# Performance work log

Hardware: AMD Instinct MI355X
Metric: run time of the kernel (lower is better)

## Reference

```python
import jax, jax.numpy as jnp
from jax import lax
import numpy as np

B, T, DIM = 2, 2048, 2048
H, Dk, Dv, K = 16, 128, 128, 4
QD, VD = H * Dk, H * Dv


def setup_inputs() -> dict:
    key = jax.random.key(0)
    ks = jax.random.split(key, 16)
    s = 0.02
    f32 = jnp.float32
    return {
        "x": jax.random.normal(ks[0], (B, T, DIM), f32),
        "Wq": jax.random.normal(ks[1], (DIM, QD), f32) * s,
        "Wk": jax.random.normal(ks[2], (DIM, QD), f32) * s,
        "Wv": jax.random.normal(ks[3], (DIM, VD), f32) * s,
        "Wo": jax.random.normal(ks[4], (VD, DIM), f32) * s,
        "Wg": jax.random.normal(ks[5], (DIM, VD), f32) * s,
        "qconv_w": jax.random.normal(ks[6], (QD, 1, K), f32) * s,
        "qconv_b": jax.random.normal(ks[7], (QD,), f32) * s,
        "kconv_w": jax.random.normal(ks[8], (QD, 1, K), f32) * s,
        "kconv_b": jax.random.normal(ks[9], (QD,), f32) * s,
        "vconv_w": jax.random.normal(ks[10], (VD, 1, K), f32) * s,
        "vconv_b": jax.random.normal(ks[11], (VD,), f32) * s,
        "beta": jax.random.normal(ks[12], (H,), f32) * 0.1,
        "A_log": jax.random.normal(ks[13], (H,), f32) * 0.1,
    }


def _causal_conv(x, w, b):
    # x: (B, T, C); depthwise causal conv, kernel K, left-pad K-1 (matches
    # Conv1d(padding=K-1, groups=C) followed by trimming the last K-1 steps).
    C = x.shape[-1]
    xp = jnp.pad(x, ((0, 0), (K - 1, 0), (0, 0))).transpose(0, 2, 1)  # (B,C,T+K-1)
    y = lax.conv_general_dilated(
        xp, w, window_strides=(1,), padding='VALID',
        feature_group_count=C, dimension_numbers=('NCH', 'OIH', 'NCH'))
    return y.transpose(0, 2, 1) + b  # (B, T, C)


def reference(x, Wq, Wk, Wv, Wo, Wg, qconv_w, qconv_b, kconv_w, kconv_b,
              vconv_w, vconv_b, beta, A_log):
    q = jax.nn.silu(_causal_conv(x @ Wq, qconv_w, qconv_b)).reshape(B, T, H, Dk)
    k = jax.nn.silu(_causal_conv(x @ Wk, kconv_w, kconv_b)).reshape(B, T, H, Dk)
    v = _causal_conv(x @ Wv, vconv_w, vconv_b).reshape(B, T, H, Dv)

    # F.normalize(k, p=2, dim=-1) with eps clamp
    k = k / jnp.maximum(jnp.linalg.norm(k, axis=-1, keepdims=True), 1e-12)

    decay = jax.nn.sigmoid(A_log)[None, :, None, None]  # (1,H,1,1)
    bet = jax.nn.sigmoid(beta)[None, :, None, None]     # (1,H,1,1)

    def step(state, qkv_t):
        q_t, k_t, v_t = qkv_t  # (B,H,Dk), (B,H,Dk), (B,H,Dv)
        state = decay * state + bet * (v_t[..., :, None] * k_t[..., None, :])
        out_t = jnp.einsum('bhvd,bhd->bhv', state, q_t)
        return state, out_t

    qT = q.transpose(1, 0, 2, 3)  # (T,B,H,Dk)
    kT = k.transpose(1, 0, 2, 3)
    vT = v.transpose(1, 0, 2, 3)
    state0 = jnp.zeros((B, H, Dv, Dk), x.dtype)
    _, outs = lax.scan(step, state0, (qT, kT, vT))  # outs: (T,B,H,Dv)

    out = outs.transpose(1, 0, 2, 3).reshape(B, T, VD)
    out = out * jax.nn.sigmoid(x @ Wg)  # output gate
    return out @ Wo
```

## Files before the change

### kernel.cpp

```cpp
#include <hip/hip_runtime.h>
#include <math.h>

#define B_   2
#define T_   2048
#define DIM_ 2048
#define H_   16

typedef __attribute__((ext_vector_type(8))) _Float16 half8;
typedef __attribute__((ext_vector_type(4))) float f32x4;

__device__ __forceinline__ float sigmoidf_(float x) { return 1.0f / (1.0f + __expf(-x)); }

__device__ __forceinline__ void gload16(const _Float16* g, _Float16* l) {
    __builtin_amdgcn_global_load_lds((const __attribute__((address_space(1))) void*)g,
                                     (__attribute__((address_space(3))) void*)l, 16, 0, 0);
}

#define VMW(n) asm volatile("s_waitcnt vmcnt(" #n ")" ::: "memory")

__device__ __forceinline__ int tsw(int row, int s) {
    return row * 72 + ((((s >> 3) ^ ((row >> 3) & 7)) << 3) | (s & 7));
}
__device__ __forceinline__ int tswb(int row, int sb) {
    return row * 72 + (((sb ^ ((row >> 3) & 7)) << 3));
}

__global__ __launch_bounds__(256) void prep(const float* __restrict__ W0,
                                            const float* __restrict__ W1,
                                            const float* __restrict__ W2,
                                            const float* __restrict__ W3,
                                            const float* __restrict__ W4,
                                            _Float16* __restrict__ wbase,
                                            const float* __restrict__ x,
                                            _Float16* __restrict__ xh)
{
    const int z = blockIdx.z;
    if (z == 5) {
        size_t blk = ((size_t)blockIdx.y * 32 + blockIdx.x) * 8192;
#pragma unroll
        for (int j = 0; j < 4; ++j) {
            size_t i = blk + (size_t)j * 2048 + (size_t)threadIdx.x * 8;
            float4 a = *(const float4*)(x + i);
            float4 b = *(const float4*)(x + i + 4);
            half8 h;
            h[0] = (_Float16)a.x; h[1] = (_Float16)a.y; h[2] = (_Float16)a.z; h[3] = (_Float16)a.w;
            h[4] = (_Float16)b.x; h[5] = (_Float16)b.y; h[6] = (_Float16)b.z; h[7] = (_Float16)b.w;
            *(half8*)(xh + i) = h;
        }
        return;
    }
    __shared__ float t[64][65];
    const float* W = z == 0 ? W0 : z == 1 ? W1 : z == 2 ? W2 : z == 3 ? W3 : W4;
    _Float16* Wt = wbase + (size_t)z * DIM_ * DIM_;
    const int c = threadIdx.x & 63;
    const int r0 = threadIdx.x >> 6;
    const int n0 = blockIdx.x * 64, k0 = blockIdx.y * 64;
#pragma unroll
    for (int i = 0; i < 16; ++i) {
        int r = i * 4 + r0;
        t[r][c] = W[(size_t)(k0 + r) * DIM_ + n0 + c];
    }
    __syncthreads();
#pragma unroll
    for (int i = 0; i < 16; ++i) {
        int r = i * 4 + r0;
        Wt[(size_t)(n0 + r) * DIM_ + k0 + c] = (_Float16)t[c][r];
    }
}

template <int BM>
__global__ __launch_bounds__(512, 1) void gemm8ph(const _Float16* __restrict__ A,
                                                  const _Float16* __restrict__ Bt,
                                                  _Float16* __restrict__ C0, _Float16* __restrict__ C1,
                                                  _Float16* __restrict__ C2, _Float16* __restrict__ C3,
                                                  int K, int nx, int cpx)
{
    constexpr int MF  = BM / 32;
    constexpr int AQ  = MF / 4;
    constexpr int ASZ = BM * 64;
    constexpr int DSZ = (BM + 256) * 64;
    __shared__ _Float16 lds[2 * DSZ];

    const int tid = threadIdx.x;
    const int lane = tid & 63, w = tid >> 6;
    const int wr = w >> 2, wc = w & 3;
    const int l15 = lane & 15, l16 = lane >> 4;

    const int bid = blockIdx.x;
    const int swz = (bid & 7) * cpx + (bid >> 3);
    const int bm = (swz / nx) * BM, bn = (swz % nx) * 256;

    const int r0 = tid >> 3;
    const int c0 = ((tid & 7) ^ (r0 & 7)) * 8;
    const _Float16* Ab = A + (size_t)(bm + r0) * K + c0;
    const _Float16* Bb = Bt + (size_t)(bn + r0) * K + c0;

#define STAGE_A(d, kt) do { _Pragma("unroll")                                    \
    for (int u = 0; u < BM / 64; ++u)                                            \
        gload16(Ab + (size_t)(u * 64) * K + (size_t)(kt) * 64,                   \
                lds + (d) * DSZ + u * 4096 + tid * 8); } while (0)
#define STAGE_B(d, h, kt) do {                                                   \
    gload16(Bb + (size_t)((h) * 128) * K + (size_t)(kt) * 64,                    \
            lds + (d) * DSZ + ASZ + (h) * 8192 + tid * 8);                       \
    gload16(Bb + (size_t)((h) * 128 + 64) * K + (size_t)(kt) * 64,               \
            lds + (d) * DSZ + ASZ + (h) * 8192 + 4096 + tid * 8); } while (0)

    int aoff[MF][2], boff[4][2];
#pragma unroll
    for (int m = 0; m < MF; ++m) {
        int R = wr * (BM / 2) + m * 16 + l15;
#pragma unroll
        for (int ks = 0; ks < 2; ++ks)
            aoff[m][ks] = R * 64 + (((ks * 4 + l16) ^ (R & 7)) * 8);
    }
#pragma unroll
    for (int n = 0; n < 4; ++n) {
        int R = wc * 64 + n * 16 + l15;
#pragma unroll
        for (int ks = 0; ks < 2; ++ks)
            boff[n][ks] = ASZ + R * 64 + (((ks * 4 + l16) ^ (R & 7)) * 8);
    }

    f32x4 acc[MF][4] = {};
    half8 bfr[4][2];
    const int nj = K >> 7;

    STAGE_A(0, 0);
    STAGE_B(0, 0, 0); STAGE_B(0, 1, 0);
    STAGE_B(1, 0, 1); STAGE_B(1, 1, 1);
    VMW(4);
    __builtin_amdgcn_s_barrier();
    __builtin_amdgcn_sched_barrier(0);

#define PH(TT, Q, STAGECODE, VMCODE) do {                                        \
    const int dB_ = (TT) * DSZ;                                                  \
    half8 af_[AQ][2];                                                            \
    if ((Q) == 0) {                                                              \
        _Pragma("unroll") for (int n_ = 0; n_ < 4; ++n_)                         \
        _Pragma("unroll") for (int ks_ = 0; ks_ < 2; ++ks_)                      \
            bfr[n_][ks_] = *(const half8*)(lds + dB_ + boff[n_][ks_]);           \
    }                                                                            \
    _Pragma("unroll") for (int a_ = 0; a_ < AQ; ++a_)                            \
    _Pragma("unroll") for (int ks_ = 0; ks_ < 2; ++ks_)                          \
        af_[a_][ks_] = *(const half8*)(lds + dB_ + aoff[(Q) * AQ + a_][ks_]);    \
    STAGECODE;                                                                   \
    __builtin_amdgcn_s_barrier();                                                \
    asm volatile("s_waitcnt lgkmcnt(0)" ::: "memory");                           \
    __builtin_amdgcn_sched_barrier(0);                                           \
    __builtin_amdgcn_s_setprio(1);                                               \
    _Pragma("unroll") for (int ks_ = 0; ks_ < 2; ++ks_)                          \
    _Pragma("unroll") for (int a_ = 0; a_ < AQ; ++a_)                            \
    _Pragma("unroll") for (int n_ = 0; n_ < 4; ++n_)                             \
        acc[(Q) * AQ + a_][n_] = __builtin_amdgcn_mfma_f32_16x16x32_f16(         \
            af_[a_][ks_], bfr[n_][ks_], acc[(Q) * AQ + a_][n_], 0, 0, 0);        \
    __builtin_amdgcn_s_setprio(0);                                               \
    __builtin_amdgcn_sched_barrier(0);                                           \
    VMCODE;                                                                      \
    __builtin_amdgcn_s_barrier();                                                \
} while (0)

    for (int j = 0; j < nj; ++j) {
        const bool pf = (j + 1 < nj);
        const int t1 = 2 * j + 1, tn0 = 2 * j + 2, tn1 = 2 * j + 3;
        PH(0, 0, { STAGE_A(1, t1); }, {});
        PH(0, 1, { if (pf) STAGE_B(0, 0, tn0); }, {});
        PH(0, 2, { if (pf) STAGE_B(0, 1, tn0); }, {});
        PH(0, 3, {}, { if (pf) { VMW(4); } else { VMW(0); } });
        PH(1, 0, { if (pf) STAGE_A(0, tn0); }, {});
        PH(1, 1, {}, {});
        PH(1, 2, { if (pf) STAGE_B(1, 0, tn1); }, {});
        PH(1, 3, { if (pf) STAGE_B(1, 1, tn1); }, { if (pf) VMW(4); });
    }
#undef PH
#undef STAGE_A
#undef STAGE_B

    const int sel = bn >> 11;
    _Float16* __restrict__ C = sel == 0 ? C0 : sel == 1 ? C1 : sel == 2 ? C2 : C3;
    const int ccol0 = bn & 2047;
    _Float16* bb = lds;
#pragma unroll
    for (int p = 0; p < 2; ++p) {
        if (p) __syncthreads();
        if (wr == p) {
#pragma unroll
            for (int m = 0; m < MF; ++m)
#pragma unroll
                for (int n = 0; n < 4; ++n)
#pragma unroll
                    for (int r = 0; r < 4; ++r)
                        bb[(m * 16 + l16 * 4 + r) * 264 + wc * 64 + n * 16 + l15] =
                            (_Float16)acc[m][n][r];
        }
        __syncthreads();
#pragma unroll
        for (int rep = 0; rep < 8; ++rep) {
            int u = rep * 512 + tid;
            int i = u >> 5, q = u & 31;
            *(half8*)(C + (size_t)(bm + p * 128 + i) * 2048 + ccol0 + q * 8) =
                *(const half8*)(bb + i * 264 + q * 8);
        }
    }
}

template <int BM, typename OT>
__global__ __launch_bounds__(512, 4) void gemmp(const _Float16* __restrict__ A,
                                                const _Float16* __restrict__ Bt,
                                                OT* __restrict__ C0, OT* __restrict__ C1,
                                                OT* __restrict__ C2, OT* __restrict__ C3,
                                                int K, int nx, int cpx)
{
    static_assert(BM == 256, "two-pass epilogue assumes BM=256");
    constexpr int BN   = 128;
    constexpr int LPT  = (BM + BN) / 128;
    constexpr int WR   = BM / 4;
    constexpr int MF   = WR / 16;
    constexpr int ASZ  = BM * 32;
    constexpr int DSZ  = (BM + BN) * 32;
    __shared__ alignas(16) char ldsraw[3 * DSZ * 2];
    _Float16* lds = reinterpret_cast<_Float16*>(ldsraw);

    const int tid = threadIdx.x;
    const int lane = tid & 63, w = tid >> 6;
    const int wr = w >> 1, wc = w & 1;
    const int l15 = lane & 15, l16 = lane >> 4;

    const int bid = blockIdx.x;
    const int swz = (bid & 7) * cpx + (bid >> 3);
    const int bm = (swz / nx) * BM, bn = (swz % nx) * BN;

    const _Float16* src[LPT];
    int ldst[LPT];
#pragma unroll
    for (int ld = 0; ld < LPT; ++ld) {
        int F = ld * 512 + tid;
        int R = F >> 2;
        int sc = (F & 3) ^ (((R >> 3) & 1) << 1);
        src[ld] = (R < BM) ? A + (size_t)(bm + R) * K + sc * 8
                           : Bt + (size_t)(bn + R - BM) * K + sc * 8;
        ldst[ld] = F * 8;
    }

    int aoff[MF], boff[4];
#pragma unroll
    for (int m = 0; m < MF; ++m) {
        int R = wr * WR + m * 16 + l15;
        aoff[m] = R * 32 + ((l16 ^ (((R >> 3) & 1) << 1)) * 8);
    }
#pragma unroll
    for (int n = 0; n < 4; ++n) {
        int R = wc * 64 + n * 16 + l15;
        boff[n] = ASZ + R * 32 + ((l16 ^ (((R >> 3) & 1) << 1)) * 8);
    }

    f32x4 acc[MF][4] = {};
    const int nt = K >> 5;

#define STAGE(kt, buf) do { _Pragma("unroll")                                  \
    for (int ld_ = 0; ld_ < LPT; ++ld_)                                        \
        gload16(src[ld_] + (size_t)(kt) * 32, lds + (buf) * DSZ + ldst[ld_]);  \
    } while (0)

    STAGE(0, 0);
    STAGE(1, 1);
    VMW(3);
    __builtin_amdgcn_s_barrier();
    __builtin_amdgcn_sched_barrier(0);

    int cb = 0, nb = 2;
    for (int t = 0; t < nt; ++t) {
        const _Float16* L = lds + cb * DSZ;
        half8 af[MF], bf[4];
#pragma unroll
        for (int m = 0; m < MF; ++m) af[m] = *(const half8*)(L + aoff[m]);
#pragma unroll
        for (int n = 0; n < 4; ++n) bf[n] = *(const half8*)(L + boff[n]);

        const bool pf = (t + 2 < nt);
        if (pf) STAGE(t + 2, nb);

        asm volatile("s_waitcnt lgkmcnt(0)" ::: "memory");
        __builtin_amdgcn_sched_barrier(0);
        __builtin_amdgcn_s_setprio(1);
#pragma unroll
        for (int m = 0; m < MF; ++m)
#pragma unroll
            for (int n = 0; n < 4; ++n)
                acc[m][n] = __builtin_amdgcn_mfma_f32_16x16x32_f16(af[m], bf[n], acc[m][n], 0, 0, 0);
        __builtin_amdgcn_s_setprio(0);
        __builtin_amdgcn_sched_barrier(0);

        if (pf) VMW(3);
        else    VMW(0);
        __builtin_amdgcn_s_barrier();
        __builtin_amdgcn_sched_barrier(0);

        cb = (cb == 2) ? 0 : cb + 1;
        nb = (nb == 2) ? 0 : nb + 1;
    }
#undef STAGE

    const int sel = bn >> 11;
    OT* __restrict__ C = sel == 0 ? C0 : sel == 1 ? C1 : sel == 2 ? C2 : C3;
    const int ccol0 = bn & 2047;
    constexpr int VE = 16 / sizeof(OT);
    constexpr int CPR = 128 / VE;
    constexpr int BW = 128 + VE;
    OT* bb = reinterpret_cast<OT*>(ldsraw);
#pragma unroll
    for (int p = 0; p < 2; ++p) {
        if (p) __syncthreads();
        if ((wr >> 1) == p) {
            const int rb = (wr & 1) * 64;
#pragma unroll
            for (int m = 0; m < MF; ++m)
#pragma unroll
                for (int n = 0; n < 4; ++n)
#pragma unroll
                    for (int r = 0; r < 4; ++r)
                        bb[(rb + m * 16 + l16 * 4 + r) * BW + wc * 64 + n * 16 + l15] =
                            (OT)acc[m][n][r];
        }
        __syncthreads();
#pragma unroll
        for (int rep = 0; rep < (128 * CPR) / 512; ++rep) {
            int u = rep * 512 + tid;
            int i = u / CPR, q = u % CPR;
            if constexpr (sizeof(OT) == 2)
                *reinterpret_cast<half8*>(C + (size_t)(bm + p * 128 + i) * 2048 + ccol0 + q * VE) =
                    *reinterpret_cast<const half8*>(bb + i * BW + q * VE);
            else
                *reinterpret_cast<float4*>(C + (size_t)(bm + p * 128 + i) * 2048 + ccol0 + q * VE) =
                    *reinterpret_cast<const float4*>(bb + i * BW + q * VE);
        }
    }
}

__global__ __launch_bounds__(256) void conv_all(const _Float16* __restrict__ pq,
                                                const _Float16* __restrict__ pk,
                                                const _Float16* __restrict__ pv,
                                                const float* __restrict__ qw,
                                                const float* __restrict__ qb,
                                                const float* __restrict__ kw,
                                                const float* __restrict__ kb,
                                                const float* __restrict__ vw,
                                                const float* __restrict__ vb,
                                                _Float16* __restrict__ qh,
                                                _Float16* __restrict__ kh,
                                                _Float16* __restrict__ vh)
{
    const int y = blockIdx.y;
    if (y == 2) {
        int lane = threadIdx.x & 63, wv = threadIdx.x >> 6;
        size_t r = (size_t)blockIdx.x * 4 + wv;
        int h = (int)(r & 15);
        size_t gr = r >> 4;
        int t = (int)(gr & (T_ - 1));
        int c0 = h * 128 + lane * 2;

        float a0 = kb[c0], a1 = kb[c0 + 1];
#pragma unroll
        for (int j = 0; j < 4; ++j) {
            int ts = t - 3 + j;
            if (ts >= 0) {
                const _Float16* p = pk + (gr - 3 + j) * DIM_ + c0;
                a0 += (float)p[0] * kw[c0 * 4 + j];
                a1 += (float)p[1] * kw[(c0 + 1) * 4 + j];
            }
        }
        a0 = a0 * sigmoidf_(a0);
        a1 = a1 * sigmoidf_(a1);
        float ss = a0 * a0 + a1 * a1;
#pragma unroll
        for (int off = 1; off < 64; off <<= 1) ss += __shfl_xor(ss, off);
        float sc = 1.0f / fmaxf(sqrtf(ss), 1e-12f);
        kh[gr * DIM_ + c0]     = (_Float16)(a0 * sc);
        kh[gr * DIM_ + c0 + 1] = (_Float16)(a1 * sc);
        return;
    }
    if (blockIdx.x >= 4096) return;
    const int act = (y == 0);
    const _Float16* xin = act ? pq : pv;
    const float* w = act ? qw : vw;
    const float* bias = act ? qb : vb;
    _Float16* yo = act ? qh : vh;

    int idx = blockIdx.x * 256 + threadIdx.x;
    int c8 = (idx & 255) * 8;
    int t = (idx >> 8) & (T_ - 1);
    int b = idx >> 19;
    const size_t rowbase = ((size_t)b * T_ + t) * DIM_ + c8;

    float4 w4[8];
    float accv[8];
#pragma unroll
    for (int u = 0; u < 8; ++u) {
        w4[u] = *(const float4*)(w + (c8 + u) * 4);
        accv[u] = bias[c8 + u];
    }
    const _Float16* xc = xin + rowbase;
#pragma unroll
    for (int j = 0; j < 4; ++j) {
        int ts = t - 3 + j;
        if (ts >= 0) {
            half8 xv = *(const half8*)(xc + (ptrdiff_t)(j - 3) * DIM_);
#pragma unroll
            for (int u = 0; u < 8; ++u)
                accv[u] += (float)xv[u] * ((const float*)&w4[u])[j];
        }
    }
    half8 o;
#pragma unroll
    for (int u = 0; u < 8; ++u) {
        float v = accv[u];
        if (act) v = v * sigmoidf_(v);
        o[u] = (_Float16)v;
    }
    *(half8*)(yo + rowbase) = o;
}

__global__ __launch_bounds__(256) void r1_kernel(const _Float16* __restrict__ kh,
                                                 const _Float16* __restrict__ vh,
                                                 const float* __restrict__ A_log,
                                                 const float* __restrict__ beta,
                                                 _Float16* __restrict__ U)
{
    const int c = blockIdx.x & 31, bh = blockIdx.x >> 5;
    const int h = bh & 15, b = bh >> 4;
    const float decay = sigmoidf_(A_log[h]);
    const float bet = sigmoidf_(beta[h]);
    const float ld = logf(decay);

    __shared__ _Float16 sm[2 * 128 * 72];
    __shared__ float pw[64];
    _Float16* kt = sm;
    _Float16* vt = sm + 128 * 72;

    const int tid = threadIdx.x;
    if (tid < 64) pw[tid] = bet * __expf(ld * (float)(63 - tid));
    __syncthreads();

    const size_t base = ((size_t)(b * T_ + c * 64) * H_ + h) * 128;
#pragma unroll
    for (int rep = 0; rep < 4; ++rep) {
        int idx = rep * 256 + tid;
        int s = idx >> 4, dq = idx & 15;
        half8 kv = *(const half8*)(kh + base + (size_t)s * DIM_ + dq * 8);
        half8 vv = *(const half8*)(vh + base + (size_t)s * DIM_ + dq * 8);
        float sc = pw[s];
#pragma unroll
        for (int j = 0; j < 8; ++j) {
            kt[tsw(dq * 8 + j, s)] = kv[j];
            vt[tsw(dq * 8 + j, s)] = (_Float16)(sc * (float)vv[j]);
        }
    }
    __syncthreads();

    const int lane = tid & 63, w = tid >> 6;
    const int l15 = lane & 15, l16 = lane >> 4;
    f32x4 acc[2][8] = {};
#pragma unroll
    for (int ks = 0; ks < 2; ++ks) {
        half8 a0 = *(const half8*)(vt + tswb(w * 32 + l15,      ks * 4 + l16));
        half8 a1 = *(const half8*)(vt + tswb(w * 32 + 16 + l15, ks * 4 + l16));
#pragma unroll
        for (int fj = 0; fj < 8; ++fj) {
            half8 bf = *(const half8*)(kt + tswb(fj * 16 + l15, ks * 4 + l16));
            acc[0][fj] = __builtin_amdgcn_mfma_f32_16x16x32_f16(a0, bf, acc[0][fj], 0, 0, 0);
            acc[1][fj] = __builtin_amdgcn_mfma_f32_16x16x32_f16(a1, bf, acc[1][fj], 0, 0, 0);
        }
    }
    __syncthreads();

    _Float16* buf = sm;
#pragma unroll
    for (int fi = 0; fi < 2; ++fi)
#pragma unroll
        for (int fj = 0; fj < 8; ++fj)
#pragma unroll
            for (int r = 0; r < 4; ++r)
                buf[(w * 32 + fi * 16 + l16 * 4 + r) * 136 + fj * 16 + l15] =
                    (_Float16)acc[fi][fj][r];
    __syncthreads();

    _Float16* Ub = U + (((size_t)blockIdx.x) << 14);
#pragma unroll
    for (int rep = 0; rep < 8; ++rep) {
        int u = rep * 256 + tid;
        int i = u >> 4, jq = u & 15;
        *(half8*)(Ub + i * 128 + jq * 8) = *(const half8*)(buf + i * 136 + jq * 8);
    }
}

__global__ __launch_bounds__(256) void r2_kernel(const _Float16* __restrict__ U,
                                                 _Float16* __restrict__ S,
                                                 const float* __restrict__ A_log)
{
    const int blk = blockIdx.x;
    const int bh = blk >> 3, part = blk & 7, h = bh & 15;
    const float decay = sigmoidf_(A_log[h]);
    const float d64 = __expf(64.0f * logf(decay));
    const size_t base = ((size_t)bh << 19) + (size_t)part * 2048 + (size_t)threadIdx.x * 8;
    const half8* Up = (const half8*)(U + base);
    half8* Sp = (half8*)(S + base);

    float st[8] = {0, 0, 0, 0, 0, 0, 0, 0};
    half8 n0 = Up[0];
    half8 n1 = Up[2048];
    for (int c = 0; c < 32; ++c) {
        half8 cur = n0;
        n0 = n1;
        if (c + 2 < 32) n1 = Up[(size_t)(c + 2) * 2048];
        half8 so;
#pragma unroll
        for (int i = 0; i < 8; ++i) {
            so[i] = (_Float16)st[i];
            st[i] = d64 * st[i] + (float)cur[i];
        }
        Sp[(size_t)c * 2048] = so;
    }
}

__global__ __launch_bounds__(256) void r3_kernel(const _Float16* __restrict__ qh,
                                                 const _Float16* __restrict__ kh,
                                                 const _Float16* __restrict__ vh,
                                                 const _Float16* __restrict__ S,
                                                 const _Float16* __restrict__ pg,
                                                 const float* __restrict__ A_log,
                                                 const float* __restrict__ beta,
                                                 _Float16* __restrict__ gated)
{
    const int c = blockIdx.x & 31, bh = blockIdx.x >> 5;
    const int h = bh & 15, b = bh >> 4;
    const float decay = sigmoidf_(A_log[h]);
    const float bet = sigmoidf_(beta[h]);
    const float ld = logf(decay);

    __shared__ _Float16 vt[128 * 72];
    __shared__ _Float16 ps[64][72];
    __shared__ _Float16 kbuf[64 * 136];
    __shared__ float e1[65];

    const int tid = threadIdx.x;
    if (tid < 65) e1[tid] = __expf(ld * (float)tid);

    const size_t base = ((size_t)(b * T_ + c * 64) * H_ + h) * 128;
#pragma unroll
    for (int rep = 0; rep < 4; ++rep) {
        int idx = rep * 256 + tid;
        int s = idx >> 4, nq = idx & 15;
        half8 vv = *(const half8*)(vh + base + (size_t)s * DIM_ + nq * 8);
        half8 kv = *(const half8*)(kh + base + (size_t)s * DIM_ + nq * 8);
#pragma unroll
        for (int j = 0; j < 8; ++j)
            vt[tsw(nq * 8 + j, s)] = vv[j];
        *(half8*)(kbuf + s * 136 + ((nq ^ (s & 7)) * 8)) = kv;
    }
    __syncthreads();

    const int lane = tid & 63, w = tid >> 6;
    const int l15 = lane & 15, l16 = lane >> 4;

    const _Float16* qrow = qh + base + (size_t)(w * 16 + l15) * DIM_;
    half8 af[4];
#pragma unroll
    for (int kd = 0; kd < 4; ++kd) af[kd] = *(const half8*)(qrow + kd * 32 + l16 * 8);

    f32x4 pacc[4] = {};
#pragma unroll
    for (int sf = 0; sf < 4; ++sf) {
        int s = sf * 16 + l15;
#pragma unroll
        for (int kd = 0; kd < 4; ++kd) {
            half8 bf = *(const half8*)(kbuf + s * 136 + (((kd * 4 + l16) ^ (s & 7)) * 8));
            pacc[sf] = __builtin_amdgcn_mfma_f32_16x16x32_f16(af[kd], bf, pacc[sf], 0, 0, 0);
        }
    }
#pragma unroll
    for (int sf = 0; sf < 4; ++sf)
#pragma unroll
        for (int r = 0; r < 4; ++r) {
            int tl = w * 16 + l16 * 4 + r;
            int s = sf * 16 + l15;
            float f = (s <= tl) ? bet * e1[tl - s] : 0.0f;
            ps[tl][s] = (_Float16)(pacc[sf][r] * f);
        }
    __syncthreads();

    half8 pf[2];
#pragma unroll
    for (int ks = 0; ks < 2; ++ks)
        pf[ks] = *(const half8*)&ps[w * 16 + l15][ks * 32 + l16 * 8];

    f32x4 acc1[8] = {};
    f32x4 acc2[8] = {};
    const _Float16* Sb = S + (((size_t)blockIdx.x) << 14);
#pragma unroll
    for (int nf = 0; nf < 8; ++nf) {
#pragma unroll
        for (int kd = 0; kd < 4; ++kd) {
            half8 bf = *(const half8*)(Sb + (size_t)(nf * 16 + l15) * 128 + kd * 32 + l16 * 8);
            acc1[nf] = __builtin_amdgcn_mfma_f32_16x16x32_f16(af[kd], bf, acc1[nf], 0, 0, 0);
        }
#pragma unroll
        for (int ks = 0; ks < 2; ++ks) {
            half8 bf = *(const half8*)(vt + tswb(nf * 16 + l15, ks * 4 + l16));
            acc2[nf] = __builtin_amdgcn_mfma_f32_16x16x32_f16(pf[ks], bf, acc2[nf], 0, 0, 0);
        }
    }
#pragma unroll
    for (int nf = 0; nf < 8; ++nf)
#pragma unroll
        for (int r = 0; r < 4; ++r) {
            int tl = w * 16 + l16 * 4 + r;
            float o = acc2[nf][r] + e1[tl + 1] * acc1[nf][r];
            kbuf[tl * 136 + nf * 16 + l15] = (_Float16)o;
        }
    __syncthreads();

#pragma unroll
    for (int rep = 0; rep < 4; ++rep) {
        int u = rep * 256 + tid;
        int tl = u >> 4, jq = u & 15;
        size_t row = (size_t)(b * T_ + c * 64 + tl);
        half8 o8 = *(const half8*)(kbuf + tl * 136 + jq * 8);
        half8 g8 = *(const half8*)(pg + row * DIM_ + h * 128 + jq * 8);
        half8 r8;
#pragma unroll
        for (int j = 0; j < 8; ++j)
            r8[j] = (_Float16)((float)o8[j] * sigmoidf_((float)g8[j]));
        *(half8*)(gated + row * DIM_ + h * 128 + jq * 8) = r8;
    }
}

extern "C" void kernel_launch(void* const* d_in, const int* in_sizes, int n_in,
                              void* d_out, int out_size, void* d_ws, size_t ws_size,
                              hipStream_t stream)
{
    const float* x     = (const float*)d_in[0];
    const float* Wq    = (const float*)d_in[1];
    const float* Wk    = (const float*)d_in[2];
    const float* Wv    = (const float*)d_in[3];
    const float* Wo    = (const float*)d_in[4];
    const float* Wg    = (const float*)d_in[5];
    const float* qw    = (const float*)d_in[6];
    const float* qb    = (const float*)d_in[7];
    const float* kw    = (const float*)d_in[8];
    const float* kb    = (const float*)d_in[9];
    const float* vw    = (const float*)d_in[10];
    const float* vb    = (const float*)d_in[11];
    const float* beta  = (const float*)d_in[12];
    const float* A_log = (const float*)d_in[13];
    float* out = (float*)d_out;

    char* wsb = (char*)d_ws;
    const size_t WT  = (size_t)DIM_ * DIM_ * 2;
    const size_t SZ  = (size_t)B_ * T_ * DIM_;
    const size_t SZH = SZ * 2;

    _Float16* wtq = (_Float16*)(wsb + 0 * WT);
    _Float16* wto = (_Float16*)(wsb + 4 * WT);
    char* pbase = wsb + 5 * WT;
    _Float16* pq = (_Float16*)(pbase + 0 * SZH);
    _Float16* pk = (_Float16*)(pbase + 1 * SZH);
    _Float16* pv = (_Float16*)(pbase + 2 * SZH);
    _Float16* xh = (_Float16*)(pbase + 3 * SZH);
    _Float16* pg = (_Float16*)(pbase + 4 * SZH);
    _Float16* qh = (_Float16*)(pbase + 5 * SZH);
    _Float16* kh = (_Float16*)(pbase + 6 * SZH);
    _Float16* vh = (_Float16*)(pbase + 7 * SZH);
    _Float16* U     = pq;
    _Float16* Sst   = pv;
    _Float16* gated = pq;

    prep<<<dim3(32, 32, 6), 256, 0, stream>>>(Wq, Wk, Wv, Wg, Wo, wtq, x, xh);

    gemm8ph<256><<<512, 512, 0, stream>>>(xh, wtq, pq, pk, pv, pg,
                                          DIM_, 32, 64);

    conv_all<<<dim3(16384, 3), 256, 0, stream>>>(pq, pk, pv,
                                                 qw, qb, kw, kb, vw, vb,
                                                 qh, kh, vh);

    r1_kernel<<<B_ * H_ * 32, 256, 0, stream>>>(kh, vh, A_log, beta, U);
    r2_kernel<<<256, 256, 0, stream>>>(U, Sst, A_log);
    r3_kernel<<<B_ * H_ * 32, 256, 0, stream>>>(qh, kh, vh, Sst, pg, A_log, beta, gated);

    gemmp<256, float><<<256, 512, 0, stream>>>(gated, wto, out, out, out, out,
                                               DIM_, 16, 32);
}
```

Measured before the change: 389.8 us.

## Fuse causal conv, SiLU and key normalization into recurrence chunk kernels

Drops the standalone conv_all kernel. The depthwise causal conv, SiLU activation and L2 normalization of k are now computed inline inside r1 and r3 from the raw projection outputs, and q is staged through a new LDS buffer. This saves a kernel launch and a full write-and-reread of the q/k/v fp16 intermediates, at the cost of doing the k/v conv twice (once in r1, once in r3) and more LDS per block in r3. The weight-transpose prep is also rewritten to use float4 loads and half8 stores.

```diff
diff --git a/kernel.cpp b/kernel.cpp
--- a/kernel.cpp
+++ b/kernel.cpp
@@ -23,6 +23,28 @@
 }
 __device__ __forceinline__ int tswb(int row, int sb) {
     return row * 72 + (((sb ^ ((row >> 3) & 7)) << 3));
+}
+
+__device__ __forceinline__ void conv8(const _Float16* __restrict__ src,
+                                      const float* __restrict__ w,
+                                      const float* __restrict__ bias,
+                                      size_t rb, int t, int ch, float* acc)
+{
+    float4 w4[8];
+#pragma unroll
+    for (int u = 0; u < 8; ++u) {
+        w4[u] = *(const float4*)(w + (ch + u) * 4);
+        acc[u] = bias[ch + u];
+    }
+#pragma unroll
+    for (int j = 0; j < 4; ++j) {
+        if (t - 3 + j >= 0) {
+            half8 xv = *(const half8*)(src + rb + (ptrdiff_t)(j - 3) * DIM_);
+#pragma unroll
+            for (int u = 0; u < 8; ++u)
+                acc[u] += (float)xv[u] * ((const float*)&w4[u])[j];
+        }
+    }
 }
 
 __global__ __launch_bounds__(256) void prep(const float* __restrict__ W0,
@@ -49,22 +71,30 @@
         }
         return;
     }
-    __shared__ float t[64][65];
+    __shared__ float t[64 * 65];
     const float* W = z == 0 ? W0 : z == 1 ? W1 : z == 2 ? W2 : z == 3 ? W3 : W4;
     _Float16* Wt = wbase + (size_t)z * DIM_ * DIM_;
-    const int c = threadIdx.x & 63;
-    const int r0 = threadIdx.x >> 6;
     const int n0 = blockIdx.x * 64, k0 = blockIdx.y * 64;
 #pragma unroll
-    for (int i = 0; i < 16; ++i) {
-        int r = i * 4 + r0;
-        t[r][c] = W[(size_t)(k0 + r) * DIM_ + n0 + c];
-    }
-    __syncthreads();
-#pragma unroll
-    for (int i = 0; i < 16; ++i) {
-        int r = i * 4 + r0;
-        Wt[(size_t)(n0 + r) * DIM_ + k0 + c] = (_Float16)t[c][r];
+    for (int rep = 0; rep < 4; ++rep) {
+        int row = rep * 16 + (threadIdx.x >> 4);
+        int qc = threadIdx.x & 15;
+        float4 v = *(const float4*)(W + (size_t)(k0 + row) * DIM_ + n0 + qc * 4);
+        t[row * 65 + qc * 4 + 0] = v.x;
+        t[row * 65 + qc * 4 + 1] = v.y;
+        t[row * 65 + qc * 4 + 2] = v.z;
+        t[row * 65 + qc * 4 + 3] = v.w;
+    }
+    __syncthreads();
+#pragma unroll
+    for (int rep = 0; rep < 2; ++rep) {
+        int r = rep * 32 + (threadIdx.x >> 3);
+        int q = threadIdx.x & 7;
+        half8 o;
+#pragma unroll
+        for (int j = 0; j < 8; ++j)
+            o[j] = (_Float16)t[(q * 8 + j) * 65 + r];
+        *(half8*)(Wt + (size_t)(n0 + r) * DIM_ + k0 + q * 8) = o;
     }
 }
 
@@ -336,91 +366,12 @@
     }
 }
 
-__global__ __launch_bounds__(256) void conv_all(const _Float16* __restrict__ pq,
-                                                const _Float16* __restrict__ pk,
-                                                const _Float16* __restrict__ pv,
-                                                const float* __restrict__ qw,
-                                                const float* __restrict__ qb,
-                                                const float* __restrict__ kw,
-                                                const float* __restrict__ kb,
-                                                const float* __restrict__ vw,
-                                                const float* __restrict__ vb,
-                                                _Float16* __restrict__ qh,
-                                                _Float16* __restrict__ kh,
-                                                _Float16* __restrict__ vh)
-{
-    const int y = blockIdx.y;
-    if (y == 2) {
-        int lane = threadIdx.x & 63, wv = threadIdx.x >> 6;
-        size_t r = (size_t)blockIdx.x * 4 + wv;
-        int h = (int)(r & 15);
-        size_t gr = r >> 4;
-        int t = (int)(gr & (T_ - 1));
-        int c0 = h * 128 + lane * 2;
-
-        float a0 = kb[c0], a1 = kb[c0 + 1];
-#pragma unroll
-        for (int j = 0; j < 4; ++j) {
-            int ts = t - 3 + j;
-            if (ts >= 0) {
-                const _Float16* p = pk + (gr - 3 + j) * DIM_ + c0;
-                a0 += (float)p[0] * kw[c0 * 4 + j];
-                a1 += (float)p[1] * kw[(c0 + 1) * 4 + j];
-            }
-        }
-        a0 = a0 * sigmoidf_(a0);
-        a1 = a1 * sigmoidf_(a1);
-        float ss = a0 * a0 + a1 * a1;
-#pragma unroll
-        for (int off = 1; off < 64; off <<= 1) ss += __shfl_xor(ss, off);
-        float sc = 1.0f / fmaxf(sqrtf(ss), 1e-12f);
-        kh[gr * DIM_ + c0]     = (_Float16)(a0 * sc);
-        kh[gr * DIM_ + c0 + 1] = (_Float16)(a1 * sc);
-        return;
-    }
-    if (blockIdx.x >= 4096) return;
-    const int act = (y == 0);
-    const _Float16* xin = act ? pq : pv;
-    const float* w = act ? qw : vw;
-    const float* bias = act ? qb : vb;
-    _Float16* yo = act ? qh : vh;
-
-    int idx = blockIdx.x * 256 + threadIdx.x;
-    int c8 = (idx & 255) * 8;
-    int t = (idx >> 8) & (T_ - 1);
-    int b = idx >> 19;
-    const size_t rowbase = ((size_t)b * T_ + t) * DIM_ + c8;
-
-    float4 w4[8];
-    float accv[8];
-#pragma unroll
-    for (int u = 0; u < 8; ++u) {
-        w4[u] = *(const float4*)(w + (c8 + u) * 4);
-        accv[u] = bias[c8 + u];
-    }
-    const _Float16* xc = xin + rowbase;
-#pragma unroll
-    for (int j = 0; j < 4; ++j) {
-        int ts = t - 3 + j;
-        if (ts >= 0) {
-            half8 xv = *(const half8*)(xc + (ptrdiff_t)(j - 3) * DIM_);
-#pragma unroll
-            for (int u = 0; u < 8; ++u)
-                accv[u] += (float)xv[u] * ((const float*)&w4[u])[j];
-        }
-    }
-    half8 o;
-#pragma unroll
-    for (int u = 0; u < 8; ++u) {
-        float v = accv[u];
-        if (act) v = v * sigmoidf_(v);
-        o[u] = (_Float16)v;
-    }
-    *(half8*)(yo + rowbase) = o;
-}
-
-__global__ __launch_bounds__(256) void r1_kernel(const _Float16* __restrict__ kh,
-                                                 const _Float16* __restrict__ vh,
+__global__ __launch_bounds__(256) void r1_kernel(const _Float16* __restrict__ pk,
+                                                 const _Float16* __restrict__ pv,
+                                                 const float* __restrict__ kw,
+                                                 const float* __restrict__ kb,
+                                                 const float* __restrict__ vw,
+                                                 const float* __restrict__ vb,
                                                  const float* __restrict__ A_log,
                                                  const float* __restrict__ beta,
                                                  _Float16* __restrict__ U)
@@ -440,18 +391,32 @@
     if (tid < 64) pw[tid] = bet * __expf(ld * (float)(63 - tid));
     __syncthreads();
 
-    const size_t base = ((size_t)(b * T_ + c * 64) * H_ + h) * 128;
 #pragma unroll
     for (int rep = 0; rep < 4; ++rep) {
-        int idx = rep * 256 + tid;
-        int s = idx >> 4, dq = idx & 15;
-        half8 kv = *(const half8*)(kh + base + (size_t)s * DIM_ + dq * 8);
-        half8 vv = *(const half8*)(vh + base + (size_t)s * DIM_ + dq * 8);
-        float sc = pw[s];
-#pragma unroll
-        for (int j = 0; j < 8; ++j) {
-            kt[tsw(dq * 8 + j, s)] = kv[j];
-            vt[tsw(dq * 8 + j, s)] = (_Float16)(sc * (float)vv[j]);
+        int s = rep * 16 + (tid >> 4);
+        int dq = tid & 15;
+        int t = c * 64 + s;
+        int ch = h * 128 + dq * 8;
+        size_t rb = ((size_t)(b * T_ + t)) * DIM_ + ch;
+        float ka[8], va[8];
+        conv8(pk, kw, kb, rb, t, ch, ka);
+        conv8(pv, vw, vb, rb, t, ch, va);
+        float ss = 0.0f;
+#pragma unroll
+        for (int u = 0; u < 8; ++u) {
+            ka[u] = ka[u] * sigmoidf_(ka[u]);
+            ss += ka[u] * ka[u];
+        }
+        ss += __shfl_xor(ss, 1);
+        ss += __shfl_xor(ss, 2);
+        ss += __shfl_xor(ss, 4);
+        ss += __shfl_xor(ss, 8);
+        float sc = 1.0f / fmaxf(sqrtf(ss), 1e-12f);
+        float vsc = pw[s];
+#pragma unroll
+        for (int u = 0; u < 8; ++u) {
+            kt[tsw(dq * 8 + u, s)] = (_Float16)(ka[u] * sc);
+            vt[tsw(dq * 8 + u, s)] = (_Float16)(vsc * va[u]);
         }
     }
     __syncthreads();
@@ -521,11 +486,17 @@
     }
 }
 
-__global__ __launch_bounds__(256) void r3_kernel(const _Float16* __restrict__ qh,
-                                                 const _Float16* __restrict__ kh,
-                                                 const _Float16* __restrict__ vh,
+__global__ __launch_bounds__(256) void r3_kernel(const _Float16* __restrict__ pq,
+                                                 const _Float16* __restrict__ pk,
+                                                 const _Float16* __restrict__ pv,
                                                  const _Float16* __restrict__ S,
                                                  const _Float16* __restrict__ pg,
+                                                 const float* __restrict__ qw,
+                                                 const float* __restrict__ qb,
+                                                 const float* __restrict__ kw,
+                                                 const float* __restrict__ kb,
+                                                 const float* __restrict__ vw,
+                                                 const float* __restrict__ vb,
                                                  const float* __restrict__ A_log,
                                                  const float* __restrict__ beta,
                                                  _Float16* __restrict__ gated)
@@ -539,32 +510,55 @@
     __shared__ _Float16 vt[128 * 72];
     __shared__ _Float16 ps[64][72];
     __shared__ _Float16 kbuf[64 * 136];
+    __shared__ _Float16 qbuf[64 * 136];
     __shared__ float e1[65];
 
     const int tid = threadIdx.x;
     if (tid < 65) e1[tid] = __expf(ld * (float)tid);
 
-    const size_t base = ((size_t)(b * T_ + c * 64) * H_ + h) * 128;
 #pragma unroll
     for (int rep = 0; rep < 4; ++rep) {
-        int idx = rep * 256 + tid;
-        int s = idx >> 4, nq = idx & 15;
-        half8 vv = *(const half8*)(vh + base + (size_t)s * DIM_ + nq * 8);
-        half8 kv = *(const half8*)(kh + base + (size_t)s * DIM_ + nq * 8);
-#pragma unroll
-        for (int j = 0; j < 8; ++j)
-            vt[tsw(nq * 8 + j, s)] = vv[j];
-        *(half8*)(kbuf + s * 136 + ((nq ^ (s & 7)) * 8)) = kv;
+        int s = rep * 16 + (tid >> 4);
+        int nq = tid & 15;
+        int t = c * 64 + s;
+        int ch = h * 128 + nq * 8;
+        size_t rb = ((size_t)(b * T_ + t)) * DIM_ + ch;
+        float qa[8], ka[8], va[8];
+        conv8(pq, qw, qb, rb, t, ch, qa);
+        conv8(pk, kw, kb, rb, t, ch, ka);
+        conv8(pv, vw, vb, rb, t, ch, va);
+        float ss = 0.0f;
+#pragma unroll
+        for (int u = 0; u < 8; ++u) {
+            qa[u] = qa[u] * sigmoidf_(qa[u]);
+            ka[u] = ka[u] * sigmoidf_(ka[u]);
+            ss += ka[u] * ka[u];
+        }
+        ss += __shfl_xor(ss, 1);
+        ss += __shfl_xor(ss, 2);
+        ss += __shfl_xor(ss, 4);
+        ss += __shfl_xor(ss, 8);
+        float sc = 1.0f / fmaxf(sqrtf(ss), 1e-12f);
+        half8 k8, q8;
+#pragma unroll
+        for (int u = 0; u < 8; ++u) {
+            k8[u] = (_Float16)(ka[u] * sc);
+            q8[u] = (_Float16)qa[u];
+            vt[tsw(nq * 8 + u, s)] = (_Float16)va[u];
+        }
+        *(half8*)(kbuf + s * 136 + ((nq ^ (s & 7)) * 8)) = k8;
+        *(half8*)(qbuf + s * 136 + ((nq ^ (s & 7)) * 8)) = q8;
     }
     __syncthreads();
 
     const int lane = tid & 63, w = tid >> 6;
     const int l15 = lane & 15, l16 = lane >> 4;
-
-    const _Float16* qrow = qh + base + (size_t)(w * 16 + l15) * DIM_;
+    const int qr = w * 16 + l15;
+
     half8 af[4];
 #pragma unroll
-    for (int kd = 0; kd < 4; ++kd) af[kd] = *(const half8*)(qrow + kd * 32 + l16 * 8);
+    for (int kd = 0; kd < 4; ++kd)
+        af[kd] = *(const half8*)(qbuf + qr * 136 + (((kd * 4 + l16) ^ (qr & 7)) * 8));
 
     f32x4 pacc[4] = {};
 #pragma unroll
@@ -666,25 +660,21 @@
     _Float16* pv = (_Float16*)(pbase + 2 * SZH);
     _Float16* xh = (_Float16*)(pbase + 3 * SZH);
     _Float16* pg = (_Float16*)(pbase + 4 * SZH);
-    _Float16* qh = (_Float16*)(pbase + 5 * SZH);
-    _Float16* kh = (_Float16*)(pbase + 6 * SZH);
-    _Float16* vh = (_Float16*)(pbase + 7 * SZH);
-    _Float16* U     = pq;
-    _Float16* Sst   = pv;
-    _Float16* gated = pq;
+    _Float16* U    = (_Float16*)(pbase + 5 * SZH);
+    _Float16* Sst  = (_Float16*)(pbase + 7 * SZH);
+    _Float16* gated = U;
 
     prep<<<dim3(32, 32, 6), 256, 0, stream>>>(Wq, Wk, Wv, Wg, Wo, wtq, x, xh);
 
     gemm8ph<256><<<512, 512, 0, stream>>>(xh, wtq, pq, pk, pv, pg,
                                           DIM_, 32, 64);
 
-    conv_all<<<dim3(16384, 3), 256, 0, stream>>>(pq, pk, pv,
-                                                 qw, qb, kw, kb, vw, vb,
-                                                 qh, kh, vh);
-
-    r1_kernel<<<B_ * H_ * 32, 256, 0, stream>>>(kh, vh, A_log, beta, U);
+    r1_kernel<<<B_ * H_ * 32, 256, 0, stream>>>(pk, pv, kw, kb, vw, vb,
+                                                A_log, beta, U);
     r2_kernel<<<256, 256, 0, stream>>>(U, Sst, A_log);
-    r3_kernel<<<B_ * H_ * 32, 256, 0, stream>>>(qh, kh, vh, Sst, pg, A_log, beta, gated);
+    r3_kernel<<<B_ * H_ * 32, 256, 0, stream>>>(pq, pk, pv, Sst, pg,
+                                                qw, qb, kw, kb, vw, vb,
+                                                A_log, beta, gated);
 
     gemmp<256, float><<<256, 512, 0, stream>>>(gated, wto, out, out, out, out,
                                                DIM_, 16, 32);
```

Measured after the change: 391.7 us. Within noise of the previous version (+0.5%).
